# Performance work log

Measured on AMD Instinct MI355X. Metric: run time of the kernel, lower is better.

## Reference

```python
import jax, jax.numpy as jnp
import numpy as np

B = 16384
LATENT = 16
HID = 512
STYLE = 64
D = 10  # num_domains


def setup_inputs() -> dict:
    key = jax.random.key(0)
    ks = jax.random.split(key, 20)
    s = 0.02
    inp = {
        "z": jax.random.normal(ks[0], (B, LATENT), jnp.float32),
        "y": jax.random.randint(ks[1], (B,), 0, D, jnp.int32),
        "W0": jax.random.normal(ks[2], (LATENT, HID), jnp.float32) * s,
        "b0": jnp.zeros((HID,), jnp.float32),
        "W1": jax.random.normal(ks[3], (HID, HID), jnp.float32) * s,
        "b1": jnp.zeros((HID,), jnp.float32),
        "W2": jax.random.normal(ks[4], (HID, HID), jnp.float32) * s,
        "b2": jnp.zeros((HID,), jnp.float32),
        "W3": jax.random.normal(ks[5], (HID, HID), jnp.float32) * s,
        "b3": jnp.zeros((HID,), jnp.float32),
        "Wu1": jax.random.normal(ks[6], (D, HID, HID), jnp.float32) * s,
        "bu1": jnp.zeros((D, HID), jnp.float32),
        "Wu2": jax.random.normal(ks[7], (D, HID, HID), jnp.float32) * s,
        "bu2": jnp.zeros((D, HID), jnp.float32),
        "Wu3": jax.random.normal(ks[8], (D, HID, HID), jnp.float32) * s,
        "bu3": jnp.zeros((D, HID), jnp.float32),
        "Wo": jax.random.normal(ks[9], (D, HID, STYLE), jnp.float32) * s,
        "bo": jnp.zeros((D, STYLE), jnp.float32),
    }
    return inp


def reference(z, y, W0, b0, W1, b1, W2, b2, W3, b3,
              Wu1, bu1, Wu2, bu2, Wu3, bu3, Wo, bo):
    # shared trunk
    h = jax.nn.relu(z @ W0 + b0)
    h = jax.nn.relu(h @ W1 + b1)
    h = jax.nn.relu(h @ W2 + b2)
    h = jax.nn.relu(h @ W3 + b3)            # [B, HID]
    # all unshared heads computed densely (as in the original torch.stack)
    t = jax.nn.relu(jnp.einsum('bh,dhk->bdk', h, Wu1) + bu1)   # [B, D, HID]
    t = jax.nn.relu(jnp.einsum('bdh,dhk->bdk', t, Wu2) + bu2)
    t = jax.nn.relu(jnp.einsum('bdh,dhk->bdk', t, Wu3) + bu3)
    out = jnp.einsum('bdh,dhk->bdk', t, Wo) + bo               # [B, D, STYLE]
    # gather the branch indexed by y for each sample
    s = out[jnp.arange(z.shape[0]), y]                          # [B, STYLE]
    return s
```

## Files before the change

### kernel.cpp

```cpp
#include <hip/hip_runtime.h>

#define NB 16384
#define NDOM 10
#define HIDN 512
#define STYLE 64
#define NWIN 512

typedef short bf16x8 __attribute__((ext_vector_type(8)));
typedef float f32x16 __attribute__((ext_vector_type(16)));

#define MFMA __builtin_amdgcn_mfma_f32_32x32x16_bf16


__device__ __forceinline__ unsigned bfr_hi(float x) {
    unsigned u = __float_as_uint(x);
    return (u + 0x7fffu + ((u >> 16) & 1u)) & 0xffff0000u;
}

__device__ __forceinline__ unsigned cvtpk(float a, float b) {
    unsigned r;
    asm("v_cvt_pk_bf16_f32 %0, %1, %2" : "=v"(r) : "v"(a), "v"(b));
    return r;
}

__device__ __forceinline__ void cvhalf2(const float4& x, const float4& y, uint4& h, uint4& l) {
    float xs[8] = {x.x, x.y, x.z, x.w, y.x, y.y, y.z, y.w};
    unsigned hh[8], ll[8];
#pragma unroll
    for (int i = 0; i < 8; ++i) {
        unsigned hb = bfr_hi(xs[i]);
        hh[i] = hb;
        ll[i] = bfr_hi(xs[i] - __uint_as_float(hb));
    }
    h = make_uint4((hh[0] >> 16) | (hh[1] & 0xffff0000u), (hh[2] >> 16) | (hh[3] & 0xffff0000u),
                   (hh[4] >> 16) | (hh[5] & 0xffff0000u), (hh[6] >> 16) | (hh[7] & 0xffff0000u));
    l = make_uint4((ll[0] >> 16) | (ll[1] & 0xffff0000u), (ll[2] >> 16) | (ll[3] & 0xffff0000u),
                   (ll[4] >> 16) | (ll[5] & 0xffff0000u), (ll[6] >> 16) | (ll[7] & 0xffff0000u));
}


__global__ void k_hist(const int* __restrict__ y, int* __restrict__ counts) {
    int b = blockIdx.x * 256 + threadIdx.x;
    int d = y[b];
    int lane = threadIdx.x & 63;
#pragma unroll
    for (int dd = 0; dd < NDOM; ++dd) {
        unsigned long long bal = __ballot(d == dd);
        if (bal != 0ULL && d == dd && lane == __builtin_ctzll(bal))
            atomicAdd(&counts[dd], (int)__popcll(bal));
    }
}

__global__ void k_scatter(const int* __restrict__ y, const int* __restrict__ counts,
                          int* __restrict__ cursors, int* __restrict__ rowidx) {
    __shared__ int soff[NDOM];
    if (threadIdx.x == 0) {
        int s = 0;
        for (int dd = 0; dd < NDOM; ++dd) { soff[dd] = s; s += counts[dd]; }
    }
    __syncthreads();
    int b = blockIdx.x * 256 + threadIdx.x;
    int d = y[b];
    int lane = threadIdx.x & 63;
#pragma unroll
    for (int dd = 0; dd < NDOM; ++dd) {
        unsigned long long bal = __ballot(d == dd);
        if (bal == 0ULL) continue;
        int leader = __builtin_ctzll(bal);
        int base = 0;
        if (d == dd && lane == leader)
            base = atomicAdd(&cursors[dd], (int)__popcll(bal));
        base = __shfl(base, leader);
        if (d == dd) {
            int rank = (int)__popcll(bal & ((1ULL << lane) - 1ULL));
            rowidx[soff[dd] + base + rank] = b;
        }
    }
}


__global__ void k_prep(const float* __restrict__ W1, const float* __restrict__ W2,
                       const float* __restrict__ W3, const float* __restrict__ Wu1,
                       const float* __restrict__ Wu2, const float* __restrict__ Wu3,
                       const float* __restrict__ W0, const float* __restrict__ Wo,
                       short* __restrict__ Wp, short* __restrict__ W0p,
                       short* __restrict__ WoP)
{
    const int b = blockIdx.x;
    const int t = threadIdx.x;
    if (b < 1056) {
        __shared__ float Ld[64][66];
        const int mat = b >> 5, wq = (b >> 2) & 7, sh = b & 3;
        const float* src;
        if (mat < 3) src = (mat == 0 ? W1 : (mat == 1 ? W2 : W3));
        else {
            int g = (mat - 3) / 10, d = (mat - 3) % 10;
            src = (g == 0 ? Wu1 : (g == 1 ? Wu2 : Wu3)) + (size_t)d * HIDN * HIDN;
        }
        short* dst = Wp + (size_t)mat * 262144 + wq * 32768;
        for (int s = sh * 2; s < sh * 2 + 2; ++s) {
            __syncthreads();
            const int r4 = t >> 6, c = t & 63;
#pragma unroll
            for (int p = 0; p < 16; ++p) {
                int k = s * 64 + p * 4 + r4;
                Ld[p * 4 + r4][c] = src[(size_t)k * HIDN + wq * 64 + c];
            }
            __syncthreads();
#pragma unroll
            for (int i = 0; i < 2; ++i) {
                int g = i * 256 + t;
                int ksl = g >> 7, of = (g >> 6) & 1, k8 = (g >> 5) & 1, c5 = g & 31;
                int kk = ksl * 16 + k8 * 8;
                unsigned pk[4];
#pragma unroll
                for (int j2 = 0; j2 < 4; ++j2) {
                    unsigned h0 = bfr_hi(Ld[kk + 2 * j2][of * 32 + c5]);
                    unsigned h1 = bfr_hi(Ld[kk + 2 * j2 + 1][of * 32 + c5]);
                    pk[j2] = (h0 >> 16) | (h1 & 0xffff0000u);
                }
                int ksg = s * 4 + ksl;
                *(uint4*)(dst + ksg * 1024 + of * 512 + k8 * 256 + c5 * 8) =
                    make_uint4(pk[0], pk[1], pk[2], pk[3]);
            }
        }
    } else if (b == 1056) {
#pragma unroll
        for (int i = 0; i < 4; ++i) {
            int g = i * 256 + t;
            int wq = g >> 7, of = (g >> 6) & 1, k8 = (g >> 5) & 1, c5 = g & 31;
            int col = wq * 64 + of * 32 + c5;
            unsigned pk[4];
#pragma unroll
            for (int j2 = 0; j2 < 4; ++j2) {
                unsigned h0 = bfr_hi(W0[(size_t)(k8 * 8 + 2 * j2) * HIDN + col]);
                unsigned h1 = bfr_hi(W0[(size_t)(k8 * 8 + 2 * j2 + 1) * HIDN + col]);
                pk[j2] = (h0 >> 16) | (h1 & 0xffff0000u);
            }
            *(uint4*)(W0p + g * 8) = make_uint4(pk[0], pk[1], pk[2], pk[3]);
        }
    } else {
        const int dom = b - 1057;
        const float* src = Wo + (size_t)dom * HIDN * STYLE;
        short* dst = WoP + (size_t)dom * 32768;
#pragma unroll
        for (int i = 0; i < 16; ++i) {
            int g = i * 256 + t;
            int w1 = g >> 11, ks = (g >> 6) & 31, k8 = (g >> 5) & 1, c5 = g & 31;
            int col = w1 * 32 + c5;
            int k0 = ks * 16 + k8 * 8;
            unsigned pk[4];
#pragma unroll
            for (int j2 = 0; j2 < 4; ++j2) {
                unsigned h0 = bfr_hi(src[(size_t)(k0 + 2 * j2) * STYLE + col]);
                unsigned h1 = bfr_hi(src[(size_t)(k0 + 2 * j2 + 1) * STYLE + col]);
                pk[j2] = (h0 >> 16) | (h1 & 0xffff0000u);
            }
            *(uint4*)(dst + g * 8) = make_uint4(pk[0], pk[1], pk[2], pk[3]);
        }
    }
}


template<bool BLO>
__device__ __forceinline__ void pass512(const short* __restrict__ sH,
                                        const short* __restrict__ sL,
                                        const short* __restrict__ pW,
                                        int w, int lane, f32x16 acc[2])
{
#pragma unroll
    for (int of = 0; of < 2; ++of)
#pragma unroll
        for (int e = 0; e < 16; ++e) acc[of][e] = 0.f;
    const int rb = (lane & 31) * 8;
    const int lh = lane >> 5;
    const short* pOf[2];
#pragma unroll
    for (int of = 0; of < 2; ++of)
        pOf[of] = pW + w * 32768 + of * 512 + lane * 8;
    bf16x8 wv[4][2];
#pragma unroll
    for (int d = 0; d < 4; ++d)
#pragma unroll
        for (int of = 0; of < 2; ++of)
            wv[d][of] = *(const bf16x8*)(pOf[of] + d * 1024);
    bf16x8 hb[2], lb[2];
    hb[0] = *(const bf16x8*)(sH + lh * 256 + rb);
    if (BLO) lb[0] = *(const bf16x8*)(sL + lh * 256 + rb);
#pragma unroll
    for (int ks = 0; ks < 32; ++ks) {
        const int pc = ks & 1, pn = pc ^ 1;
        bf16x8 wk[2];
        wk[0] = wv[ks & 3][0];
        wk[1] = wv[ks & 3][1];
        if (ks < 28) {
            wv[ks & 3][0] = *(const bf16x8*)(pOf[0] + (ks + 4) * 1024);
            wv[ks & 3][1] = *(const bf16x8*)(pOf[1] + (ks + 4) * 1024);
        }
        if (ks < 31) {
            const int basen = (2 * (ks + 1) + lh) * 256 + rb;
            hb[pn] = *(const bf16x8*)(sH + basen);
            if (BLO) lb[pn] = *(const bf16x8*)(sL + basen);
        }
        acc[0] = MFMA(wk[0], hb[pc], acc[0], 0, 0, 0);
        acc[1] = MFMA(wk[1], hb[pc], acc[1], 0, 0, 0);
        if (BLO) {
            acc[0] = MFMA(wk[0], lb[pc], acc[0], 0, 0, 0);
            acc[1] = MFMA(wk[1], lb[pc], acc[1], 0, 0, 0);
        }
    }
}

template<bool WLO, bool RELU>
__device__ __forceinline__ void epi512(short* __restrict__ sH, short* __restrict__ sL,
                                       f32x16 acc[2],
                                       const float* __restrict__ bias,
                                       int w, int lane, int rlo, int rhi)
{
    const int lh = lane >> 5;
    const int row = lane & 31;
    const bool pred = (row >= rlo && row < rhi);
#pragma unroll
    for (int of = 0; of < 2; ++of) {
        unsigned mh[4][2], ml[4][2];
#pragma unroll
        for (int q = 0; q < 4; ++q) {
            const float4 bv = *(const float4*)&bias[(w * 2 + of) * 32 + q * 8 + lh * 4];
            float v[4];
#pragma unroll
            for (int j = 0; j < 4; ++j) {
                float x = acc[of][q * 4 + j] + (&bv.x)[j];
                if (RELU) x = fmaxf(x, 0.f);
                v[j] = x;
            }
            mh[q][0] = cvtpk(v[0], v[1]);
            mh[q][1] = cvtpk(v[2], v[3]);
            if (WLO) {
                float l0 = v[0] - __uint_as_float(mh[q][0] << 16);
                float l1 = v[1] - __uint_as_float(mh[q][0] & 0xffff0000u);
                float l2 = v[2] - __uint_as_float(mh[q][1] << 16);
                float l3 = v[3] - __uint_as_float(mh[q][1] & 0xffff0000u);
                ml[q][0] = cvtpk(l0, l1);
                ml[q][1] = cvtpk(l2, l3);
            }
        }
#pragma unroll
        for (int t = 0; t < 2; ++t) {
            const int q = 2 * t + lh;
            const int qs = 2 * t + (lh ^ 1);
            unsigned r0 = (unsigned)__shfl_xor((int)mh[qs][0], 32);
            unsigned r1 = (unsigned)__shfl_xor((int)mh[qs][1], 32);
            uint4 line = lh == 0 ? make_uint4(mh[q][0], mh[q][1], r0, r1)
                                 : make_uint4(r0, r1, mh[q][0], mh[q][1]);
            const int o = (w * 2 + of) * 4 + q;
            if (pred) *(uint4*)(sH + o * 256 + row * 8) = line;
            if (WLO) {
                unsigned s0 = (unsigned)__shfl_xor((int)ml[qs][0], 32);
                unsigned s1 = (unsigned)__shfl_xor((int)ml[qs][1], 32);
                uint4 lin2 = lh == 0 ? make_uint4(ml[q][0], ml[q][1], s0, s1)
                                     : make_uint4(s0, s1, ml[q][0], ml[q][1]);
                if (pred) *(uint4*)(sL + o * 256 + row * 8) = lin2;
            }
        }
    }
}

__global__ __launch_bounds__(512, 4)
void k_fused(const float* __restrict__ z, const int* __restrict__ rowidx,
             const int* __restrict__ counts,
             const short* __restrict__ Wp, const short* __restrict__ W0p,
             const short* __restrict__ WoP,
             const float* __restrict__ b0, const float* __restrict__ b1,
             const float* __restrict__ b2, const float* __restrict__ b3,
             const float* __restrict__ bu1, const float* __restrict__ bu2,
             const float* __restrict__ bu3, const float* __restrict__ bo,
             float* __restrict__ out)
{
    __shared__ short sH[16384];
    __shared__ short sL[16384];
    __shared__ int soff[NDOM + 1];

    const int win = (blockIdx.x & 7) * 64 + (blockIdx.x >> 3);
    const int row0 = win * 32;
    const int tid = threadIdx.x;
    const int lane = tid & 63;
    const int w = tid >> 6;
    const int lh = lane >> 5;

    if (tid == 0) {
        int s = 0;
#pragma unroll
        for (int dd = 0; dd < NDOM; ++dd) { soff[dd] = s; s += counts[dd]; }
        soff[NDOM] = s;
    }

    f32x16 acc[2];

    {
#pragma unroll
        for (int of = 0; of < 2; ++of)
#pragma unroll
            for (int e = 0; e < 16; ++e) acc[of][e] = 0.f;
        bf16x8 w0v[2];
#pragma unroll
        for (int of = 0; of < 2; ++of)
            w0v[of] = *(const bf16x8*)(W0p + w * 1024 + of * 512 + lane * 8);
        const int r = lane & 31;
        const int src = rowidx[row0 + r];
        const float* zp = z + (size_t)src * 16 + lh * 8;
        float4 f0 = *(const float4*)zp;
        float4 f1 = *(const float4*)(zp + 4);
        uint4 h, l;
        cvhalf2(f0, f1, h, l);
        bf16x8 zh = *(bf16x8*)&h;
        bf16x8 zl = *(bf16x8*)&l;
        acc[0] = MFMA(w0v[0], zh, acc[0], 0, 0, 0);
        acc[1] = MFMA(w0v[1], zh, acc[1], 0, 0, 0);
        acc[0] = MFMA(w0v[0], zl, acc[0], 0, 0, 0);
        acc[1] = MFMA(w0v[1], zl, acc[1], 0, 0, 0);
        epi512<false, true>(sH, sL, acc, b0, w, lane, 0, 32);
        __syncthreads();
    }

#pragma unroll 1
    for (int m = 0; m < 3; ++m) {
        const float* bp = (m == 0) ? b1 : (m == 1) ? b2 : b3;
        pass512<false>(sH, sL, Wp + (size_t)m * 262144, w, lane, acc);
        __syncthreads();
        if (m < 2) epi512<false, true>(sH, sL, acc, bp, w, lane, 0, 32);
        else       epi512<true,  true>(sH, sL, acc, bp, w, lane, 0, 32);
        __syncthreads();
    }

#pragma unroll 1
    for (int L = 0; L < 3; ++L) {
        const short* WL_ = Wp + (size_t)(3 + L * 10) * 262144;
        const float* bL = (L == 0) ? bu1 : (L == 1) ? bu2 : bu3;
#pragma unroll 1
        for (int d = 0; d < NDOM; ++d) {
            int rlo = soff[d] - row0, rhi = soff[d + 1] - row0;
            rlo = rlo < 0 ? 0 : rlo;
            rhi = rhi > 32 ? 32 : rhi;
            if (rhi <= rlo) continue;
            pass512<true>(sH, sL, WL_ + (size_t)d * 262144, w, lane, acc);
            __syncthreads();
            epi512<true, true>(sH, sL, acc, bL + d * HIDN, w, lane, rlo, rhi);
            __syncthreads();
        }
    }

    if (w < 2) {
        const int r = lane & 31;
#pragma unroll 1
        for (int d = 0; d < NDOM; ++d) {
            int rlo = soff[d] - row0, rhi = soff[d + 1] - row0;
            rlo = rlo < 0 ? 0 : rlo;
            rhi = rhi > 32 ? 32 : rhi;
            if (rhi <= rlo) continue;
            f32x16 fh, fl;
#pragma unroll
            for (int e = 0; e < 16; ++e) { fh[e] = 0.f; fl[e] = 0.f; }
            const short* pw = WoP + (size_t)d * 32768 + w * 16384 + lane * 8;
            bf16x8 wb[4];
#pragma unroll
            for (int dd = 0; dd < 4; ++dd) wb[dd] = *(const bf16x8*)(pw + dd * 512);
#pragma unroll
            for (int ks = 0; ks < 32; ++ks) {
                bf16x8 wk = wb[ks & 3];
                if (ks < 28) wb[ks & 3] = *(const bf16x8*)(pw + (ks + 4) * 512);
                const int base = (2 * ks + lh) * 256 + (lane & 31) * 8;
                bf16x8 bhv = *(const bf16x8*)(sH + base);
                bf16x8 blv = *(const bf16x8*)(sL + base);
                fh = MFMA(wk, bhv, fh, 0, 0, 0);
                fl = MFMA(wk, blv, fl, 0, 0, 0);
            }
            if (r >= rlo && r < rhi) {
                const int orow = rowidx[row0 + r];
                float* op = out + (size_t)orow * STYLE + w * 32 + lh * 4;
                const float* bop = bo + d * STYLE + w * 32 + lh * 4;
#pragma unroll
                for (int q = 0; q < 4; ++q) {
                    float4 v;
                    v.x = fh[q * 4 + 0] + fl[q * 4 + 0] + bop[q * 8 + 0];
                    v.y = fh[q * 4 + 1] + fl[q * 4 + 1] + bop[q * 8 + 1];
                    v.z = fh[q * 4 + 2] + fl[q * 4 + 2] + bop[q * 8 + 2];
                    v.w = fh[q * 4 + 3] + fl[q * 4 + 3] + bop[q * 8 + 3];
                    *(float4*)(op + q * 8) = v;
                }
            }
        }
    }
}


extern "C" void kernel_launch(void* const* d_in, const int* in_sizes, int n_in,
                              void* d_out, int out_size, void* d_ws, size_t ws_size,
                              hipStream_t stream) {
    const float* z   = (const float*)d_in[0];
    const int*   y   = (const int*)d_in[1];
    const float* W0  = (const float*)d_in[2];
    const float* b0  = (const float*)d_in[3];
    const float* W1  = (const float*)d_in[4];
    const float* b1  = (const float*)d_in[5];
    const float* W2  = (const float*)d_in[6];
    const float* b2  = (const float*)d_in[7];
    const float* W3  = (const float*)d_in[8];
    const float* b3  = (const float*)d_in[9];
    const float* Wu1 = (const float*)d_in[10];
    const float* bu1 = (const float*)d_in[11];
    const float* Wu2 = (const float*)d_in[12];
    const float* bu2 = (const float*)d_in[13];
    const float* Wu3 = (const float*)d_in[14];
    const float* bu3 = (const float*)d_in[15];
    const float* Wo  = (const float*)d_in[16];
    const float* bo  = (const float*)d_in[17];
    float* out = (float*)d_out;

    short* Wp   = (short*)d_ws;
    short* W0p  = Wp + (size_t)33 * 262144;
    short* WoP  = W0p + 8192;
    int* rowidx  = (int*)(WoP + (size_t)10 * 32768);
    int* counts  = rowidx + NB;
    int* cursors = counts + NDOM;

    hipMemsetAsync(counts, 0, sizeof(int) * 2 * NDOM, stream);
    k_hist<<<NB / 256, 256, 0, stream>>>(y, counts);
    k_scatter<<<NB / 256, 256, 0, stream>>>(y, counts, cursors, rowidx);
    k_prep<<<1067, 256, 0, stream>>>(W1, W2, W3, Wu1, Wu2, Wu3, W0, Wo, Wp, W0p, WoP);
    k_fused<<<NWIN, 512, 0, stream>>>(z, rowidx, counts, Wp, W0p, WoP,
                                      b0, b1, b2, b3, bu1, bu2, bu3, bo, out);
}
```

Before: 195.4 us.

## Double fused-kernel wavefronts to one output tile each; fold histogram into prep

The fused MLP kernel now runs 16 wavefronts per 1024-thread block, each computing a single 32-column MFMA output tile instead of two. That halves per-wave accumulator and weight-prefetch registers and doubles the waves available to hide latency. The domain histogram kernel is merged into the weight-prep launch as extra blocks, removing one kernel launch. The risk is more barrier cost per block, and the unseen head/output section must also be adapted to 16 waves.

Measured after the change: 209.4 us. 1.07x slower.

```diff
diff --git a/kernel.cpp b/kernel.cpp
--- a/kernel.cpp
+++ b/kernel.cpp
@@ -38,18 +38,6 @@
                    (ll[4] >> 16) | (ll[5] & 0xffff0000u), (ll[6] >> 16) | (ll[7] & 0xffff0000u));
 }
 
-
-__global__ void k_hist(const int* __restrict__ y, int* __restrict__ counts) {
-    int b = blockIdx.x * 256 + threadIdx.x;
-    int d = y[b];
-    int lane = threadIdx.x & 63;
-#pragma unroll
-    for (int dd = 0; dd < NDOM; ++dd) {
-        unsigned long long bal = __ballot(d == dd);
-        if (bal != 0ULL && d == dd && lane == __builtin_ctzll(bal))
-            atomicAdd(&counts[dd], (int)__popcll(bal));
-    }
-}
 
 __global__ void k_scatter(const int* __restrict__ y, const int* __restrict__ counts,
                           int* __restrict__ cursors, int* __restrict__ rowidx) {
@@ -83,8 +71,9 @@
                        const float* __restrict__ W3, const float* __restrict__ Wu1,
                        const float* __restrict__ Wu2, const float* __restrict__ Wu3,
                        const float* __restrict__ W0, const float* __restrict__ Wo,
+                       const int* __restrict__ y,
                        short* __restrict__ Wp, short* __restrict__ W0p,
-                       short* __restrict__ WoP)
+                       short* __restrict__ WoP, int* __restrict__ counts)
 {
     const int b = blockIdx.x;
     const int t = threadIdx.x;
@@ -139,7 +128,7 @@
             }
             *(uint4*)(W0p + g * 8) = make_uint4(pk[0], pk[1], pk[2], pk[3]);
         }
-    } else {
+    } else if (b < 1067) {
         const int dom = b - 1057;
         const float* src = Wo + (size_t)dom * HIDN * STYLE;
         short* dst = WoP + (size_t)dom * 32768;
@@ -158,6 +147,16 @@
             }
             *(uint4*)(dst + g * 8) = make_uint4(pk[0], pk[1], pk[2], pk[3]);
         }
+    } else {
+        int idx = (b - 1067) * 256 + t;
+        int d = y[idx];
+        int lane = t & 63;
+#pragma unroll
+        for (int dd = 0; dd < NDOM; ++dd) {
+            unsigned long long bal = __ballot(d == dd);
+            if (bal != 0ULL && d == dd && lane == __builtin_ctzll(bal))
+                atomicAdd(&counts[dd], (int)__popcll(bal));
+        }
     }
 }
 
@@ -166,106 +165,86 @@
 __device__ __forceinline__ void pass512(const short* __restrict__ sH,
                                         const short* __restrict__ sL,
                                         const short* __restrict__ pW,
-                                        int w, int lane, f32x16 acc[2])
+                                        int w, int lane, f32x16& acc)
 {
 #pragma unroll
-    for (int of = 0; of < 2; ++of)
-#pragma unroll
-        for (int e = 0; e < 16; ++e) acc[of][e] = 0.f;
+    for (int e = 0; e < 16; ++e) acc[e] = 0.f;
     const int rb = (lane & 31) * 8;
     const int lh = lane >> 5;
-    const short* pOf[2];
-#pragma unroll
-    for (int of = 0; of < 2; ++of)
-        pOf[of] = pW + w * 32768 + of * 512 + lane * 8;
-    bf16x8 wv[4][2];
-#pragma unroll
-    for (int d = 0; d < 4; ++d)
-#pragma unroll
-        for (int of = 0; of < 2; ++of)
-            wv[d][of] = *(const bf16x8*)(pOf[of] + d * 1024);
+    const short* p = pW + (w >> 1) * 32768 + (w & 1) * 512 + lane * 8;
+    bf16x8 wv[4];
+#pragma unroll
+    for (int d = 0; d < 4; ++d) wv[d] = *(const bf16x8*)(p + d * 1024);
     bf16x8 hb[2], lb[2];
     hb[0] = *(const bf16x8*)(sH + lh * 256 + rb);
     if (BLO) lb[0] = *(const bf16x8*)(sL + lh * 256 + rb);
 #pragma unroll
     for (int ks = 0; ks < 32; ++ks) {
         const int pc = ks & 1, pn = pc ^ 1;
-        bf16x8 wk[2];
-        wk[0] = wv[ks & 3][0];
-        wk[1] = wv[ks & 3][1];
-        if (ks < 28) {
-            wv[ks & 3][0] = *(const bf16x8*)(pOf[0] + (ks + 4) * 1024);
-            wv[ks & 3][1] = *(const bf16x8*)(pOf[1] + (ks + 4) * 1024);
-        }
+        bf16x8 wk = wv[ks & 3];
+        if (ks < 28) wv[ks & 3] = *(const bf16x8*)(p + (ks + 4) * 1024);
         if (ks < 31) {
             const int basen = (2 * (ks + 1) + lh) * 256 + rb;
             hb[pn] = *(const bf16x8*)(sH + basen);
             if (BLO) lb[pn] = *(const bf16x8*)(sL + basen);
         }
-        acc[0] = MFMA(wk[0], hb[pc], acc[0], 0, 0, 0);
-        acc[1] = MFMA(wk[1], hb[pc], acc[1], 0, 0, 0);
-        if (BLO) {
-            acc[0] = MFMA(wk[0], lb[pc], acc[0], 0, 0, 0);
-            acc[1] = MFMA(wk[1], lb[pc], acc[1], 0, 0, 0);
-        }
+        acc = MFMA(wk, hb[pc], acc, 0, 0, 0);
+        if (BLO) acc = MFMA(wk, lb[pc], acc, 0, 0, 0);
     }
 }
 
 template<bool WLO, bool RELU>
 __device__ __forceinline__ void epi512(short* __restrict__ sH, short* __restrict__ sL,
-                                       f32x16 acc[2],
+                                       f32x16& acc,
                                        const float* __restrict__ bias,
                                        int w, int lane, int rlo, int rhi)
 {
     const int lh = lane >> 5;
     const int row = lane & 31;
     const bool pred = (row >= rlo && row < rhi);
-#pragma unroll
-    for (int of = 0; of < 2; ++of) {
-        unsigned mh[4][2], ml[4][2];
-#pragma unroll
-        for (int q = 0; q < 4; ++q) {
-            const float4 bv = *(const float4*)&bias[(w * 2 + of) * 32 + q * 8 + lh * 4];
-            float v[4];
-#pragma unroll
-            for (int j = 0; j < 4; ++j) {
-                float x = acc[of][q * 4 + j] + (&bv.x)[j];
-                if (RELU) x = fmaxf(x, 0.f);
-                v[j] = x;
-            }
-            mh[q][0] = cvtpk(v[0], v[1]);
-            mh[q][1] = cvtpk(v[2], v[3]);
-            if (WLO) {
-                float l0 = v[0] - __uint_as_float(mh[q][0] << 16);
-                float l1 = v[1] - __uint_as_float(mh[q][0] & 0xffff0000u);
-                float l2 = v[2] - __uint_as_float(mh[q][1] << 16);
-                float l3 = v[3] - __uint_as_float(mh[q][1] & 0xffff0000u);
-                ml[q][0] = cvtpk(l0, l1);
-                ml[q][1] = cvtpk(l2, l3);
-            }
-        }
-#pragma unroll
-        for (int t = 0; t < 2; ++t) {
-            const int q = 2 * t + lh;
-            const int qs = 2 * t + (lh ^ 1);
-            unsigned r0 = (unsigned)__shfl_xor((int)mh[qs][0], 32);
-            unsigned r1 = (unsigned)__shfl_xor((int)mh[qs][1], 32);
-            uint4 line = lh == 0 ? make_uint4(mh[q][0], mh[q][1], r0, r1)
-                                 : make_uint4(r0, r1, mh[q][0], mh[q][1]);
-            const int o = (w * 2 + of) * 4 + q;
-            if (pred) *(uint4*)(sH + o * 256 + row * 8) = line;
-            if (WLO) {
-                unsigned s0 = (unsigned)__shfl_xor((int)ml[qs][0], 32);
-                unsigned s1 = (unsigned)__shfl_xor((int)ml[qs][1], 32);
-                uint4 lin2 = lh == 0 ? make_uint4(ml[q][0], ml[q][1], s0, s1)
-                                     : make_uint4(s0, s1, ml[q][0], ml[q][1]);
-                if (pred) *(uint4*)(sL + o * 256 + row * 8) = lin2;
-            }
-        }
-    }
-}
-
-__global__ __launch_bounds__(512, 4)
+    unsigned mh[4][2], ml[4][2];
+#pragma unroll
+    for (int q = 0; q < 4; ++q) {
+        const float4 bv = *(const float4*)&bias[w * 32 + q * 8 + lh * 4];
+        float v[4];
+#pragma unroll
+        for (int j = 0; j < 4; ++j) {
+            float x = acc[q * 4 + j] + (&bv.x)[j];
+            if (RELU) x = fmaxf(x, 0.f);
+            v[j] = x;
+        }
+        mh[q][0] = cvtpk(v[0], v[1]);
+        mh[q][1] = cvtpk(v[2], v[3]);
+        if (WLO) {
+            float l0 = v[0] - __uint_as_float(mh[q][0] << 16);
+            float l1 = v[1] - __uint_as_float(mh[q][0] & 0xffff0000u);
+            float l2 = v[2] - __uint_as_float(mh[q][1] << 16);
+            float l3 = v[3] - __uint_as_float(mh[q][1] & 0xffff0000u);
+            ml[q][0] = cvtpk(l0, l1);
+            ml[q][1] = cvtpk(l2, l3);
+        }
+    }
+#pragma unroll
+    for (int t = 0; t < 2; ++t) {
+        const int q = 2 * t + lh;
+        const int qs = 2 * t + (lh ^ 1);
+        unsigned r0 = (unsigned)__shfl_xor((int)mh[qs][0], 32);
+        unsigned r1 = (unsigned)__shfl_xor((int)mh[qs][1], 32);
+        uint4 line = lh == 0 ? make_uint4(mh[q][0], mh[q][1], r0, r1)
+                             : make_uint4(r0, r1, mh[q][0], mh[q][1]);
+        const int o = w * 4 + q;
+        if (pred) *(uint4*)(sH + o * 256 + row * 8) = line;
+        if (WLO) {
+            unsigned s0 = (unsigned)__shfl_xor((int)ml[qs][0], 32);
+            unsigned s1 = (unsigned)__shfl_xor((int)ml[qs][1], 32);
+            uint4 lin2 = lh == 0 ? make_uint4(ml[q][0], ml[q][1], s0, s1)
+                                 : make_uint4(s0, s1, ml[q][0], ml[q][1]);
+            if (pred) *(uint4*)(sL + o * 256 + row * 8) = lin2;
+        }
+    }
+}
+
+__global__ __launch_bounds__(1024, 8)
 void k_fused(const float* __restrict__ z, const int* __restrict__ rowidx,
              const int* __restrict__ counts,
              const short* __restrict__ Wp, const short* __restrict__ W0p,
@@ -294,17 +273,12 @@
         soff[NDOM] = s;
     }
 
-    f32x16 acc[2];
+    f32x16 acc;
 
     {
 #pragma unroll
-        for (int of = 0; of < 2; ++of)
-#pragma unroll
-            for (int e = 0; e < 16; ++e) acc[of][e] = 0.f;
-        bf16x8 w0v[2];
-#pragma unroll
-        for (int of = 0; of < 2; ++of)
-            w0v[of] = *(const bf16x8*)(W0p + w * 1024 + of * 512 + lane * 8);
+        for (int e = 0; e < 16; ++e) acc[e] = 0.f;
+        bf16x8 w0v = *(const bf16x8*)(W0p + (w >> 1) * 1024 + (w & 1) * 512 + lane * 8);
         const int r = lane & 31;
         const int src = rowidx[row0 + r];
         const float* zp = z + (size_t)src * 16 + lh * 8;
@@ -314,10 +288,8 @@
         cvhalf2(f0, f1, h, l);
         bf16x8 zh = *(bf16x8*)&h;
         bf16x8 zl = *(bf16x8*)&l;
-        acc[0] = MFMA(w0v[0], zh, acc[0], 0, 0, 0);
-        acc[1] = MFMA(w0v[1], zh, acc[1], 0, 0, 0);
-        acc[0] = MFMA(w0v[0], zl, acc[0], 0, 0, 0);
-        acc[1] = MFMA(w0v[1], zl, acc[1], 0, 0, 0);
+        acc = MFMA(w0v, zh, acc, 0, 0, 0);
+        acc = MFMA(w0v, zl, acc, 0, 0, 0);
         epi512<false, true>(sH, sL, acc, b0, w, lane, 0, 32);
         __syncthreads();
     }
@@ -424,9 +396,9 @@
     int* cursors = counts + NDOM;
 
     hipMemsetAsync(counts, 0, sizeof(int) * 2 * NDOM, stream);
-    k_hist<<<NB / 256, 256, 0, stream>>>(y, counts);
+    k_prep<<<1131, 256, 0, stream>>>(W1, W2, W3, Wu1, Wu2, Wu3, W0, Wo, y,
+                                     Wp, W0p, WoP, counts);
     k_scatter<<<NB / 256, 256, 0, stream>>>(y, counts, cursors, rowidx);
-    k_prep<<<1067, 256, 0, stream>>>(W1, W2, W3, Wu1, Wu2, Wu3, W0, Wo, Wp, W0p, WoP);
-    k_fused<<<NWIN, 512, 0, stream>>>(z, rowidx, counts, Wp, W0p, WoP,
-                                      b0, b1, b2, b3, bu1, bu2, bu3, bo, out);
-}
+    k_fused<<<NWIN, 1024, 0, stream>>>(z, rowidx, counts, Wp, W0p, WoP,
+                                       b0, b1, b2, b3, bu1, bu2, bu3, bo, out);
+}
```
